# Performance work log

Hardware: AMD Instinct MI355X
Metric: run time of the kernel (lower is better)

The kernel has to match this reference:

```python
import jax, jax.numpy as jnp
import numpy as np

N_NODES = 100000
N_EDGES = 1600000
F_IN = 256
HID = 128
N_CLS = 64
K_APPNP = 10
ALPHA = 0.1


def setup_inputs() -> dict:
    key = jax.random.key(0)
    ks = jax.random.split(key, 12)
    x = jax.random.normal(ks[0], (N_NODES, F_IN), dtype=jnp.float32)
    edge_index = jax.random.randint(ks[1], (2, N_EDGES), 0, N_NODES, dtype=jnp.int64)
    def lin(k, fan_in, fan_out):
        s = 1.0 / np.sqrt(fan_in)
        kw, kb = jax.random.split(k)
        W = jax.random.uniform(kw, (fan_in, fan_out), minval=-s, maxval=s, dtype=jnp.float32)
        b = jax.random.uniform(kb, (fan_out,), minval=-s, maxval=s, dtype=jnp.float32)
        return W, b
    W1, b1 = lin(ks[2], F_IN, HID)
    W2, b2 = lin(ks[3], HID, HID)
    Wc, bc = lin(ks[4], HID, N_CLS)
    We, be = lin(ks[5], N_CLS, N_CLS)
    return {"x": x, "edge_index": edge_index, "W1": W1, "b1": b1, "W2": W2,
            "b2": b2, "Wc": Wc, "bc": bc, "We": We, "be": be}


def reference(x, edge_index, W1, b1, W2, b2, Wc, bc, We, be):
    N = x.shape[0]
    loop = jnp.arange(N)
    row = jnp.concatenate([edge_index[0], loop])  # source nodes (+ self loops)
    col = jnp.concatenate([edge_index[1], loop])  # target nodes (+ self loops)
    # symmetric GCN normalization: deg computed on targets
    deg = jax.ops.segment_sum(jnp.ones_like(col, dtype=x.dtype), col, num_segments=N)
    dinv = jnp.where(deg > 0, jax.lax.rsqrt(deg), 0.0)
    norm = dinv[row] * dinv[col]  # [E+N]

    def prop(h):  # normalized scatter-add aggregation
        return jax.ops.segment_sum(h[row] * norm[:, None], col, num_segments=N)

    # GCNConv: transform -> propagate -> bias (dropout is eval no-op)
    h = jax.nn.relu(prop(x @ W1) + b1)
    h = jax.nn.relu(prop(h @ W2) + b2)
    logits = h @ Wc + bc
    ev = jax.nn.relu(logits @ We + be)
    # APPNP: z_{k+1} = (1-alpha) * A_hat z_k + alpha * ev
    z = ev
    for _ in range(K_APPNP):
        z = (1.0 - ALPHA) * prop(z) + ALPHA * ev
    return jax.nn.log_softmax(z, axis=1)
```

## Files before the change

### kernel.cpp

```cpp
#include <hip/hip_runtime.h>
#include <hip/hip_fp16.h>


struct __align__(16) half8 { __half2 h[4]; };
typedef _Float16 f16x8 __attribute__((ext_vector_type(8)));
typedef float f32x4 __attribute__((ext_vector_type(4)));

__global__ __launch_bounds__(256) void k_init(int* deg, int N) {
    int i = blockIdx.x * 256 + threadIdx.x;
    if (i < N) deg[i] = 1;
}

__global__ __launch_bounds__(256) void k_count(const int* __restrict__ dst,
                                               int* deg, int* __restrict__ rank, int E) {
    int e = blockIdx.x * 256 + threadIdx.x;
    if (e < E) {
        int r = atomicAdd(&deg[dst[e]], 1);
        rank[e] = r - 1;
    }
}

__global__ __launch_bounds__(256) void k_scanA(const int* __restrict__ deg, int* bs, int N) {
    __shared__ int s[256];
    int t = threadIdx.x;
    int i = blockIdx.x * 256 + t;
    int c = (i < N) ? (deg[i] - 1) : 0;
    s[t] = c; __syncthreads();
    for (int o = 128; o > 0; o >>= 1) {
        if (t < o) s[t] += s[t + o];
        __syncthreads();
    }
    if (t == 0) bs[blockIdx.x] = s[0];
}

__global__ __launch_bounds__(512) void k_scanB(int* bs, int NB) {
    __shared__ int s[512];
    int t = threadIdx.x;
    int v = (t < NB) ? bs[t] : 0;
    s[t] = v; __syncthreads();
    for (int o = 1; o < 512; o <<= 1) {
        int u = (t >= o) ? s[t - o] : 0;
        __syncthreads();
        s[t] += u;
        __syncthreads();
    }
    if (t < NB) bs[t] = s[t] - v;
}

__global__ __launch_bounds__(256) void k_scanC(const int* __restrict__ deg, const int* __restrict__ bs,
                                               int* row_ptr, float* dinv, int N) {
    __shared__ int s[256];
    int t = threadIdx.x;
    int i = blockIdx.x * 256 + t;
    int c = (i < N) ? (deg[i] - 1) : 0;
    s[t] = c; __syncthreads();
    for (int o = 1; o < 256; o <<= 1) {
        int u = (t >= o) ? s[t - o] : 0;
        __syncthreads();
        s[t] += u;
        __syncthreads();
    }
    if (i < N) {
        int off = bs[blockIdx.x];
        row_ptr[i] = off + s[t] - c;
        dinv[i] = rsqrtf((float)deg[i]);
        if (i == N - 1) row_ptr[N] = off + s[t];
    }
}

__global__ __launch_bounds__(256) void k_fill(const int* __restrict__ src, const int* __restrict__ dst,
                                              const int* __restrict__ row_ptr,
                                              const int* __restrict__ rank,
                                              int* __restrict__ csr_src, int E) {
    int e = blockIdx.x * 256 + threadIdx.x;
    if (e < E) csr_src[row_ptr[dst[e]] + rank[e]] = src[e];
}

__global__ __launch_bounds__(256) void k_fuseW(const float* __restrict__ Wc,
                                               const float* __restrict__ bc,
                                               const float* __restrict__ We,
                                               const float* __restrict__ be,
                                               float* __restrict__ Wf,
                                               float* __restrict__ bf) {
    __shared__ float sWe[64 * 64];
    int tid = threadIdx.x;
    for (int i = tid; i < 64 * 64 / 4; i += 256)
        ((float4*)sWe)[i] = ((const float4*)We)[i];
    __syncthreads();
    for (int idx = tid; idx < 128 * 64; idx += 256) {
        int r = idx >> 6, c = idx & 63;
        float s = 0.f;
#pragma unroll 8
        for (int j = 0; j < 64; j++) s += Wc[r * 64 + j] * sWe[j * 64 + c];
        Wf[idx] = s;
    }
    if (tid < 64) {
        float s = be[tid];
#pragma unroll 8
        for (int j = 0; j < 64; j++) s += bc[j] * sWe[j * 64 + tid];
        bf[tid] = s;
    }
}

__global__ __launch_bounds__(256) void k_prepW(const float* __restrict__ W,
                                               __half* __restrict__ Wt, int K, int NCOL) {
    int idx = blockIdx.x * 256 + threadIdx.x;
    if (idx < NCOL * K) {
        int n = idx / K, k = idx % K;
        Wt[idx] = __float2half(W[k * NCOL + n]);
    }
}

template <int K, bool IN_F16>
__global__ __launch_bounds__(256) void k_mfma_gemm(const void* __restrict__ Xv,
                                                   const __half* __restrict__ Wt,
                                                   const float* __restrict__ dinv,
                                                   __half* __restrict__ Y, int N) {
    constexpr int NK = K / 32;
    const int tid = threadIdx.x;
    const int wave = tid >> 6, lane = tid & 63;
    const int m = lane & 15, quad = lane >> 4;
    const int rw = (wave & 1) * 16;
    const int cb = (wave >> 1) * 64;
    const int rowBase = blockIdx.x * 32;
    int rowA = rowBase + rw + m;
    if (rowA > N - 1) rowA = N - 1;

    const float*  xf = (const float*)Xv;
    const __half* xh = (const __half*)Xv;
    const long aOff = (long)rowA * K + quad * 8;

    f32x4 d[4];
#pragma unroll
    for (int ct = 0; ct < 4; ++ct) d[ct] = {0.f, 0.f, 0.f, 0.f};

    f16x8 a[2];
    float4 t0[2], t1[2];
    f16x8 b[2][4];

    if constexpr (IN_F16) {
        a[0] = *(const f16x8*)&xh[aOff];
    } else {
        t0[0] = *(const float4*)&xf[aOff];
        t1[0] = *(const float4*)&xf[aOff + 4];
    }
#pragma unroll
    for (int ct = 0; ct < 4; ++ct)
        b[0][ct] = *(const f16x8*)&Wt[(long)(cb + ct * 16 + m) * K + quad * 8];

#pragma unroll
    for (int kc = 0; kc < NK; ++kc) {
        const int cur = kc & 1, nxt = cur ^ 1;
        if (kc + 1 < NK) {
            const int k1 = (kc + 1) * 32;
            if constexpr (IN_F16) {
                a[nxt] = *(const f16x8*)&xh[aOff + k1];
            } else {
                t0[nxt] = *(const float4*)&xf[aOff + k1];
                t1[nxt] = *(const float4*)&xf[aOff + k1 + 4];
            }
#pragma unroll
            for (int ct = 0; ct < 4; ++ct)
                b[nxt][ct] = *(const f16x8*)&Wt[(long)(cb + ct * 16 + m) * K + k1 + quad * 8];
        }
        if constexpr (!IN_F16) {
            f16x8 av;
            av[0] = (_Float16)t0[cur].x; av[1] = (_Float16)t0[cur].y;
            av[2] = (_Float16)t0[cur].z; av[3] = (_Float16)t0[cur].w;
            av[4] = (_Float16)t1[cur].x; av[5] = (_Float16)t1[cur].y;
            av[6] = (_Float16)t1[cur].z; av[7] = (_Float16)t1[cur].w;
            a[cur] = av;
        }
#pragma unroll
        for (int ct = 0; ct < 4; ++ct)
            d[ct] = __builtin_amdgcn_mfma_f32_16x16x32_f16(a[cur], b[cur][ct], d[ct], 0, 0, 0);
    }

#pragma unroll
    for (int ct = 0; ct < 4; ++ct) {
        const int col = cb + ct * 16 + m;
#pragma unroll
        for (int reg = 0; reg < 4; ++reg) {
            const int row = rowBase + rw + quad * 4 + reg;
            if (row < N)
                Y[(long)row * 128 + col] = __float2half(d[ct][reg] * dinv[row]);
        }
    }
}

__global__ __launch_bounds__(256) void k_cls(const __half* __restrict__ H,
                                             const __half* __restrict__ Wft,
                                             const float* __restrict__ bf,
                                             const float* __restrict__ dinv,
                                             float* __restrict__ ev,
                                             __half* __restrict__ evs, int N) {
    const int tid = threadIdx.x;
    const int wave = tid >> 6, lane = tid & 63;
    const int m = lane & 15, quad = lane >> 4;
    const int rowT = blockIdx.x * 64 + wave * 16;
    int rowA = rowT + m;
    if (rowA > N - 1) rowA = N - 1;
    const long aOff = (long)rowA * 128 + quad * 8;

    f32x4 d[4];
#pragma unroll
    for (int ct = 0; ct < 4; ++ct) d[ct] = {0.f, 0.f, 0.f, 0.f};

    f16x8 a[2], b[2][4];
    a[0] = *(const f16x8*)&H[aOff];
#pragma unroll
    for (int ct = 0; ct < 4; ++ct)
        b[0][ct] = *(const f16x8*)&Wft[(long)(ct * 16 + m) * 128 + quad * 8];

#pragma unroll
    for (int kc = 0; kc < 4; ++kc) {
        const int cur = kc & 1, nxt = cur ^ 1;
        if (kc + 1 < 4) {
            const int k1 = (kc + 1) * 32;
            a[nxt] = *(const f16x8*)&H[aOff + k1];
#pragma unroll
            for (int ct = 0; ct < 4; ++ct)
                b[nxt][ct] = *(const f16x8*)&Wft[(long)(ct * 16 + m) * 128 + k1 + quad * 8];
        }
#pragma unroll
        for (int ct = 0; ct < 4; ++ct)
            d[ct] = __builtin_amdgcn_mfma_f32_16x16x32_f16(a[cur], b[cur][ct], d[ct], 0, 0, 0);
    }

#pragma unroll
    for (int ct = 0; ct < 4; ++ct) {
        const int col = ct * 16 + m;
#pragma unroll
        for (int reg = 0; reg < 4; ++reg) {
            const int row = rowT + quad * 4 + reg;
            if (row < N) {
                float v = fmaxf(d[ct][reg] + bf[col], 0.f);
                ev[(long)row * 64 + col] = v;
                evs[(long)row * 64 + col] = __float2half(v * dinv[row]);
            }
        }
    }
}

template <int F, int MODE>
__global__ __launch_bounds__(256) void k_prop2(const __half* __restrict__ tab,
                                               const int* __restrict__ row_ptr,
                                               const int* __restrict__ csr_src,
                                               const float* __restrict__ dinv,
                                               const float* __restrict__ bias,
                                               const void* __restrict__ evx,
                                               void* __restrict__ out, int N) {
    constexpr int LPE = F / 8;
    constexpr int S = 64 / LPE;
    int wave = threadIdx.x >> 6;
    int lane = threadIdx.x & 63;
    int node = blockIdx.x * 4 + wave;
    if (node >= N) return;
    int slot = lane / LPE;
    int fl = lane % LPE;
    const int2 se = *(const int2*)&row_ptr[node];
    int s = se.x, e = se.y;

    float acc[8], accB[8];
#pragma unroll
    for (int q = 0; q < 8; q++) { acc[q] = 0.f; accB[q] = 0.f; }

    int j = s + slot;
    int i0 = 0, i1 = 0;
    if (j < e) i0 = csr_src[j];
    if (j + S < e) i1 = csr_src[j + S];
    while (j + S < e) {
        const int jn = j + 2 * S;
        int n0 = 0, n1 = 0;
        if (jn < e) n0 = csr_src[jn];
        if (jn + S < e) n1 = csr_src[jn + S];
        const half8 a = *(const half8*)&tab[(long)i0 * F + 8 * fl];
        const half8 b = *(const half8*)&tab[(long)i1 * F + 8 * fl];
#pragma unroll
        for (int q = 0; q < 4; q++) {
            float2 fa = __half22float2(a.h[q]);
            float2 fb = __half22float2(b.h[q]);
            acc[2 * q] += fa.x; acc[2 * q + 1] += fa.y;
            accB[2 * q] += fb.x; accB[2 * q + 1] += fb.y;
        }
        i0 = n0; i1 = n1; j = jn;
    }
    if (j < e) {
        const half8 a = *(const half8*)&tab[(long)i0 * F + 8 * fl];
#pragma unroll
        for (int q = 0; q < 4; q++) {
            float2 fa = __half22float2(a.h[q]);
            acc[2 * q] += fa.x; acc[2 * q + 1] += fa.y;
        }
    }
    if (slot == 0) {
        const half8 a = *(const half8*)&tab[(long)node * F + 8 * fl];
#pragma unroll
        for (int q = 0; q < 4; q++) {
            float2 fa = __half22float2(a.h[q]);
            acc[2 * q] += fa.x; acc[2 * q + 1] += fa.y;
        }
    }
#pragma unroll
    for (int q = 0; q < 8; q++) acc[q] += accB[q];

#pragma unroll
    for (int off = LPE; off < 64; off <<= 1) {
#pragma unroll
        for (int q = 0; q < 8; q++) acc[q] += __shfl_xor(acc[q], off, 64);
    }

    if (slot == 0) {
        float di = dinv[node];
        if (MODE == 3) {
            const float4 b0 = *(const float4*)&bias[8 * fl];
            const float4 b1 = *(const float4*)&bias[8 * fl + 4];
            half8 ov;
            ov.h[0] = __floats2half2_rn(fmaxf(di * acc[0] + b0.x, 0.f),
                                        fmaxf(di * acc[1] + b0.y, 0.f));
            ov.h[1] = __floats2half2_rn(fmaxf(di * acc[2] + b0.z, 0.f),
                                        fmaxf(di * acc[3] + b0.w, 0.f));
            ov.h[2] = __floats2half2_rn(fmaxf(di * acc[4] + b1.x, 0.f),
                                        fmaxf(di * acc[5] + b1.y, 0.f));
            ov.h[3] = __floats2half2_rn(fmaxf(di * acc[6] + b1.z, 0.f),
                                        fmaxf(di * acc[7] + b1.w, 0.f));
            *(half8*)&((__half*)out)[(long)node * F + 8 * fl] = ov;
        } else if (MODE == 1) {
            float d2 = 0.9f * di * di;
            const half8 eh = *(const half8*)&((const __half*)evx)[(long)node * F + 8 * fl];
            half8 ov;
#pragma unroll
            for (int q = 0; q < 4; q++) {
                float2 ef = __half22float2(eh.h[q]);
                float vx = d2 * acc[2 * q] + 0.1f * ef.x;
                float vy = d2 * acc[2 * q + 1] + 0.1f * ef.y;
                ov.h[q] = __floats2half2_rn(vx, vy);
            }
            *(half8*)&((__half*)out)[(long)node * F + 8 * fl] = ov;
        } else {
            float d1 = 0.9f * di;
            const float* ef = (const float*)evx + (long)node * F + 8 * fl;
            const float4 e0 = *(const float4*)ef;
            const float4 e1 = *(const float4*)(ef + 4);
            float v[8];
            v[0] = d1 * acc[0] + 0.1f * e0.x;
            v[1] = d1 * acc[1] + 0.1f * e0.y;
            v[2] = d1 * acc[2] + 0.1f * e0.z;
            v[3] = d1 * acc[3] + 0.1f * e0.w;
            v[4] = d1 * acc[4] + 0.1f * e1.x;
            v[5] = d1 * acc[5] + 0.1f * e1.y;
            v[6] = d1 * acc[6] + 0.1f * e1.z;
            v[7] = d1 * acc[7] + 0.1f * e1.w;
            float m = v[0];
#pragma unroll
            for (int q = 1; q < 8; q++) m = fmaxf(m, v[q]);
#pragma unroll
            for (int off = 1; off < LPE; off <<= 1) m = fmaxf(m, __shfl_xor(m, off, 64));
            float ssum = 0.f;
#pragma unroll
            for (int q = 0; q < 8; q++) ssum += __expf(v[q] - m);
#pragma unroll
            for (int off = 1; off < LPE; off <<= 1) ssum += __shfl_xor(ssum, off, 64);
            float lse = m + __logf(ssum);
            float* o = (float*)out + (long)node * F + 8 * fl;
            float4 v0, v1;
            v0.x = v[0] - lse; v0.y = v[1] - lse; v0.z = v[2] - lse; v0.w = v[3] - lse;
            v1.x = v[4] - lse; v1.y = v[5] - lse; v1.z = v[6] - lse; v1.w = v[7] - lse;
            *(float4*)o = v0;
            *(float4*)(o + 4) = v1;
        }
    }
}

extern "C" void kernel_launch(void* const* d_in, const int* in_sizes, int n_in,
                              void* d_out, int out_size, void* d_ws, size_t ws_size,
                              hipStream_t stream) {
    const float* x  = (const float*)d_in[0];
    const int* edges = (const int*)d_in[1];
    const float* W1 = (const float*)d_in[2];
    const float* b1 = (const float*)d_in[3];
    const float* W2 = (const float*)d_in[4];
    const float* b2 = (const float*)d_in[5];
    const float* Wc = (const float*)d_in[6];
    const float* bc = (const float*)d_in[7];
    const float* We = (const float*)d_in[8];
    const float* be = (const float*)d_in[9];

    const int N = in_sizes[0] / 256;
    const int E = in_sizes[1] / 2;
    const int* esrc = edges;
    const int* edst = edges + E;

    char* ws = (char*)d_ws;
    size_t off = 0;
    auto alloc = [&](size_t bytes) -> void* {
        void* p = ws + off;
        off += (bytes + 255) & ~(size_t)255;
        return p;
    };
    int*    deg     = (int*)alloc((size_t)N * 4);
    int*    row_ptr = (int*)alloc((size_t)(N + 1) * 4);
    float*  dinv    = (float*)alloc((size_t)N * 4);
    int*    bs      = (int*)alloc(4096 * 4);
    int*    rank    = (int*)alloc((size_t)E * 4);
    int*    csr_src = (int*)alloc((size_t)E * 4);
    __half* P       = (__half*)alloc((size_t)N * 128 * 2);
    __half* Q16     = (__half*)alloc((size_t)N * 128 * 2);
    __half* zA      = (__half*)alloc((size_t)N * 64 * 2);
    __half* zB      = (__half*)alloc((size_t)N * 64 * 2);
    __half* evs     = (__half*)alloc((size_t)N * 64 * 2);
    float*  Wf      = (float*)alloc(128 * 64 * 4);
    float*  bf      = (float*)alloc(64 * 4);
    __half* W1t     = (__half*)alloc(128 * 256 * 2);
    __half* W2t     = (__half*)alloc(128 * 128 * 2);
    __half* Wft     = (__half*)alloc(64 * 128 * 2);
    float*  ev      = (float*)d_out;

    const int nbN = (N + 255) / 256;
    const int nbE = (E + 255) / 256;
    const int nbP = (N + 3) / 4;
    const int nbG = (N + 31) / 32;
    const int nbC = (N + 63) / 64;

    k_init<<<nbN, 256, 0, stream>>>(deg, N);
    k_count<<<nbE, 256, 0, stream>>>(edst, deg, rank, E);
    k_fuseW<<<1, 256, 0, stream>>>(Wc, bc, We, be, Wf, bf);
    k_prepW<<<(128 * 256 + 255) / 256, 256, 0, stream>>>(W1, W1t, 256, 128);
    k_prepW<<<(128 * 128 + 255) / 256, 256, 0, stream>>>(W2, W2t, 128, 128);
    k_prepW<<<(64 * 128 + 255) / 256, 256, 0, stream>>>(Wf, Wft, 128, 64);
    k_scanA<<<nbN, 256, 0, stream>>>(deg, bs, N);
    k_scanB<<<1, 512, 0, stream>>>(bs, nbN);
    k_scanC<<<nbN, 256, 0, stream>>>(deg, bs, row_ptr, dinv, N);
    k_fill<<<nbE, 256, 0, stream>>>(esrc, edst, row_ptr, rank, csr_src, E);

    k_mfma_gemm<256, false><<<nbG, 256, 0, stream>>>(x, W1t, dinv, P, N);
    k_prop2<128, 3><<<nbP, 256, 0, stream>>>(P, row_ptr, csr_src, dinv, b1, nullptr, Q16, N);

    k_mfma_gemm<128, true><<<nbG, 256, 0, stream>>>(Q16, W2t, dinv, P, N);
    k_prop2<128, 3><<<nbP, 256, 0, stream>>>(P, row_ptr, csr_src, dinv, b2, nullptr, Q16, N);

    k_cls<<<nbC, 256, 0, stream>>>(Q16, Wft, bf, dinv, ev, evs, N);

    const __half* zin = evs;
    __half* zout;
    for (int it = 0; it < 9; ++it) {
        zout = (it % 2 == 0) ? zA : zB;
        k_prop2<64, 1><<<nbP, 256, 0, stream>>>(zin, row_ptr, csr_src, dinv, nullptr, evs, zout, N);
        zin = zout;
    }
    k_prop2<64, 2><<<nbP, 256, 0, stream>>>(zin, row_ptr, csr_src, dinv, nullptr, ev, (float*)d_out, N);
}
```

Before: 1.030 ms.

## Stage weights in LDS with fragment-ordered layout and enlarge GEMM row tiles

Weight matrices are pre-permuted into an MFMA-fragment-ordered layout and loaded once per block into shared memory, instead of each wave re-reading them from global memory. The GEMM and classifier kernels now use 512-thread blocks covering 128 rows, with each wave computing all output columns for its 16 rows, and all A fragments are loaded up front. This aims to reduce redundant global weight traffic and improve latency hiding in the dense stages. In exchange it adds LDS use (up to 64KB for K=256) and more registers per thread, which may limit occupancy.

```diff
diff --git a/kernel.cpp b/kernel.cpp
--- a/kernel.cpp
+++ b/kernel.cpp
@@ -5,6 +5,13 @@
 struct __align__(16) half8 { __half2 h[4]; };
 typedef _Float16 f16x8 __attribute__((ext_vector_type(8)));
 typedef float f32x4 __attribute__((ext_vector_type(4)));
+
+__device__ __forceinline__ f16x8 cvt8(const float4& a, const float4& b) {
+    f16x8 r;
+    r[0] = (_Float16)a.x; r[1] = (_Float16)a.y; r[2] = (_Float16)a.z; r[3] = (_Float16)a.w;
+    r[4] = (_Float16)b.x; r[5] = (_Float16)b.y; r[6] = (_Float16)b.z; r[7] = (_Float16)b.w;
+    return r;
+}
 
 __global__ __launch_bounds__(256) void k_init(int* deg, int N) {
     int i = blockIdx.x * 256 + threadIdx.x;
@@ -102,129 +109,153 @@
     }
 }
 
-__global__ __launch_bounds__(256) void k_prepW(const float* __restrict__ W,
-                                               __half* __restrict__ Wt, int K, int NCOL) {
+__global__ __launch_bounds__(256) void k_prepW2(const float* __restrict__ W,
+                                                __half* __restrict__ Wt, int K, int NCOL) {
     int idx = blockIdx.x * 256 + threadIdx.x;
-    if (idx < NCOL * K) {
-        int n = idx / K, k = idx % K;
-        Wt[idx] = __float2half(W[k * NCOL + n]);
-    }
+    if (idx >= K * NCOL) return;
+    int j = idx & 7;
+    int n = (idx >> 3) % NCOL;
+    int qk = idx / (8 * NCOL);
+    int quad = qk & 3, kc = qk >> 2;
+    int k = kc * 32 + quad * 8 + j;
+    Wt[idx] = __float2half(W[k * NCOL + n]);
 }
 
 template <int K, bool IN_F16>
-__global__ __launch_bounds__(256) void k_mfma_gemm(const void* __restrict__ Xv,
-                                                   const __half* __restrict__ Wt,
-                                                   const float* __restrict__ dinv,
-                                                   __half* __restrict__ Y, int N) {
+__global__ __launch_bounds__(512, 4) void k_gemm(const void* __restrict__ Xv,
+                                                 const __half* __restrict__ Wtf,
+                                                 const float* __restrict__ dinv,
+                                                 __half* __restrict__ Y, int N) {
     constexpr int NK = K / 32;
+    constexpr int ITER = K / 32;
+    __shared__ __align__(16) __half sB[K * 128];
+
     const int tid = threadIdx.x;
-    const int wave = tid >> 6, lane = tid & 63;
-    const int m = lane & 15, quad = lane >> 4;
-    const int rw = (wave & 1) * 16;
-    const int cb = (wave >> 1) * 64;
-    const int rowBase = blockIdx.x * 32;
-    int rowA = rowBase + rw + m;
+    const int wv = tid >> 6, ln = tid & 63;
+    const int m = ln & 15, quad = ln >> 4;
+    const int rowBase = blockIdx.x * 128 + wv * 16;
+    int rowA = rowBase + m;
     if (rowA > N - 1) rowA = N - 1;
 
     const float*  xf = (const float*)Xv;
     const __half* xh = (const __half*)Xv;
     const long aOff = (long)rowA * K + quad * 8;
 
-    f32x4 d[4];
-#pragma unroll
-    for (int ct = 0; ct < 4; ++ct) d[ct] = {0.f, 0.f, 0.f, 0.f};
-
-    f16x8 a[2];
-    float4 t0[2], t1[2];
-    f16x8 b[2][4];
-
+    f16x8 a8[4];
+    float4 t0[4], t1[4];
     if constexpr (IN_F16) {
-        a[0] = *(const f16x8*)&xh[aOff];
+#pragma unroll
+        for (int kc = 0; kc < NK; ++kc)
+            a8[kc] = *(const f16x8*)&xh[aOff + kc * 32];
     } else {
-        t0[0] = *(const float4*)&xf[aOff];
-        t1[0] = *(const float4*)&xf[aOff + 4];
-    }
-#pragma unroll
-    for (int ct = 0; ct < 4; ++ct)
-        b[0][ct] = *(const f16x8*)&Wt[(long)(cb + ct * 16 + m) * K + quad * 8];
-
-#pragma unroll
-    for (int kc = 0; kc < NK; ++kc) {
-        const int cur = kc & 1, nxt = cur ^ 1;
-        if (kc + 1 < NK) {
-            const int k1 = (kc + 1) * 32;
-            if constexpr (IN_F16) {
-                a[nxt] = *(const f16x8*)&xh[aOff + k1];
-            } else {
-                t0[nxt] = *(const float4*)&xf[aOff + k1];
-                t1[nxt] = *(const float4*)&xf[aOff + k1 + 4];
+#pragma unroll
+        for (int c = 0; c < 4; ++c) {
+            t0[c] = *(const float4*)&xf[aOff + c * 32];
+            t1[c] = *(const float4*)&xf[aOff + c * 32 + 4];
+        }
+    }
+
+    {
+        f16x8 tb[ITER];
+        const f16x8* g = (const f16x8*)Wtf;
+#pragma unroll
+        for (int i = 0; i < ITER; ++i) tb[i] = g[(i * 8 + wv) * 64 + ln];
+        f16x8* l = (f16x8*)sB;
+#pragma unroll
+        for (int i = 0; i < ITER; ++i) l[(i * 8 + wv) * 64 + ln] = tb[i];
+    }
+    __syncthreads();
+
+    if constexpr (!IN_F16) {
+#pragma unroll
+        for (int c = 0; c < 4; ++c) a8[c] = cvt8(t0[c], t1[c]);
+#pragma unroll
+        for (int c = 0; c < 4; ++c) {
+            t0[c] = *(const float4*)&xf[aOff + (c + 4) * 32];
+            t1[c] = *(const float4*)&xf[aOff + (c + 4) * 32 + 4];
+        }
+    }
+
+    f32x4 d[8];
+#pragma unroll
+    for (int ct = 0; ct < 8; ++ct) d[ct] = {0.f, 0.f, 0.f, 0.f};
+
+#pragma unroll
+    for (int h = 0; h < NK / 4; ++h) {
+        if constexpr (!IN_F16) {
+            if (h == 1) {
+#pragma unroll
+                for (int c = 0; c < 4; ++c) a8[c] = cvt8(t0[c], t1[c]);
             }
-#pragma unroll
-            for (int ct = 0; ct < 4; ++ct)
-                b[nxt][ct] = *(const f16x8*)&Wt[(long)(cb + ct * 16 + m) * K + k1 + quad * 8];
-        }
-        if constexpr (!IN_F16) {
-            f16x8 av;
-            av[0] = (_Float16)t0[cur].x; av[1] = (_Float16)t0[cur].y;
-            av[2] = (_Float16)t0[cur].z; av[3] = (_Float16)t0[cur].w;
-            av[4] = (_Float16)t1[cur].x; av[5] = (_Float16)t1[cur].y;
-            av[6] = (_Float16)t1[cur].z; av[7] = (_Float16)t1[cur].w;
-            a[cur] = av;
-        }
-#pragma unroll
-        for (int ct = 0; ct < 4; ++ct)
-            d[ct] = __builtin_amdgcn_mfma_f32_16x16x32_f16(a[cur], b[cur][ct], d[ct], 0, 0, 0);
-    }
-
-#pragma unroll
-    for (int ct = 0; ct < 4; ++ct) {
-        const int col = cb + ct * 16 + m;
+        }
+#pragma unroll
+        for (int kq = 0; kq < 4; ++kq) {
+            const int kc = h * 4 + kq;
+            const f16x8 a = a8[IN_F16 ? kc : kq];
+            const __half* bb = &sB[(size_t)(kc * 4 + quad) * 128 * 8];
+#pragma unroll
+            for (int ct = 0; ct < 8; ++ct) {
+                const f16x8 b = *(const f16x8*)&bb[(ct * 16 + m) * 8];
+                d[ct] = __builtin_amdgcn_mfma_f32_16x16x32_f16(a, b, d[ct], 0, 0, 0);
+            }
+        }
+    }
+
+#pragma unroll
+    for (int ct = 0; ct < 8; ++ct) {
+        const int col = ct * 16 + m;
 #pragma unroll
         for (int reg = 0; reg < 4; ++reg) {
-            const int row = rowBase + rw + quad * 4 + reg;
+            const int row = rowBase + quad * 4 + reg;
             if (row < N)
                 Y[(long)row * 128 + col] = __float2half(d[ct][reg] * dinv[row]);
         }
     }
 }
 
-__global__ __launch_bounds__(256) void k_cls(const __half* __restrict__ H,
-                                             const __half* __restrict__ Wft,
-                                             const float* __restrict__ bf,
-                                             const float* __restrict__ dinv,
-                                             float* __restrict__ ev,
-                                             __half* __restrict__ evs, int N) {
+__global__ __launch_bounds__(512, 4) void k_cls(const __half* __restrict__ H,
+                                                const __half* __restrict__ Wtf,
+                                                const float* __restrict__ bf,
+                                                const float* __restrict__ dinv,
+                                                float* __restrict__ ev,
+                                                __half* __restrict__ evs, int N) {
+    __shared__ __align__(16) __half sB[128 * 64];
     const int tid = threadIdx.x;
-    const int wave = tid >> 6, lane = tid & 63;
-    const int m = lane & 15, quad = lane >> 4;
-    const int rowT = blockIdx.x * 64 + wave * 16;
-    int rowA = rowT + m;
+    const int wv = tid >> 6, ln = tid & 63;
+    const int m = ln & 15, quad = ln >> 4;
+    const int rowBase = blockIdx.x * 128 + wv * 16;
+    int rowA = rowBase + m;
     if (rowA > N - 1) rowA = N - 1;
     const long aOff = (long)rowA * 128 + quad * 8;
 
+    f16x8 a8[4];
+#pragma unroll
+    for (int kc = 0; kc < 4; ++kc)
+        a8[kc] = *(const f16x8*)&H[aOff + kc * 32];
+
+    {
+        f16x8 tb[2];
+        const f16x8* g = (const f16x8*)Wtf;
+#pragma unroll
+        for (int i = 0; i < 2; ++i) tb[i] = g[(i * 8 + wv) * 64 + ln];
+        f16x8* l = (f16x8*)sB;
+#pragma unroll
+        for (int i = 0; i < 2; ++i) l[(i * 8 + wv) * 64 + ln] = tb[i];
+    }
+    __syncthreads();
+
     f32x4 d[4];
 #pragma unroll
     for (int ct = 0; ct < 4; ++ct) d[ct] = {0.f, 0.f, 0.f, 0.f};
 
-    f16x8 a[2], b[2][4];
-    a[0] = *(const f16x8*)&H[aOff];
-#pragma unroll
-    for (int ct = 0; ct < 4; ++ct)
-        b[0][ct] = *(const f16x8*)&Wft[(long)(ct * 16 + m) * 128 + quad * 8];
-
 #pragma unroll
     for (int kc = 0; kc < 4; ++kc) {
-        const int cur = kc & 1, nxt = cur ^ 1;
-        if (kc + 1 < 4) {
-            const int k1 = (kc + 1) * 32;
-            a[nxt] = *(const f16x8*)&H[aOff + k1];
-#pragma unroll
-            for (int ct = 0; ct < 4; ++ct)
-                b[nxt][ct] = *(const f16x8*)&Wft[(long)(ct * 16 + m) * 128 + k1 + quad * 8];
-        }
-#pragma unroll
-        for (int ct = 0; ct < 4; ++ct)
-            d[ct] = __builtin_amdgcn_mfma_f32_16x16x32_f16(a[cur], b[cur][ct], d[ct], 0, 0, 0);
+        const __half* bb = &sB[(size_t)(kc * 4 + quad) * 64 * 8];
+#pragma unroll
+        for (int ct = 0; ct < 4; ++ct) {
+            const f16x8 b = *(const f16x8*)&bb[(ct * 16 + m) * 8];
+            d[ct] = __builtin_amdgcn_mfma_f32_16x16x32_f16(a8[kc], b, d[ct], 0, 0, 0);
+        }
     }
 
 #pragma unroll
@@ -232,7 +263,7 @@
         const int col = ct * 16 + m;
 #pragma unroll
         for (int reg = 0; reg < 4; ++reg) {
-            const int row = rowT + quad * 4 + reg;
+            const int row = rowBase + quad * 4 + reg;
             if (row < N) {
                 float v = fmaxf(d[ct][reg] + bf[col], 0.f);
                 ev[(long)row * 64 + col] = v;
@@ -419,27 +450,26 @@
     const int nbN = (N + 255) / 256;
     const int nbE = (E + 255) / 256;
     const int nbP = (N + 3) / 4;
-    const int nbG = (N + 31) / 32;
-    const int nbC = (N + 63) / 64;
+    const int TG  = (N + 127) / 128;
 
     k_init<<<nbN, 256, 0, stream>>>(deg, N);
     k_count<<<nbE, 256, 0, stream>>>(edst, deg, rank, E);
     k_fuseW<<<1, 256, 0, stream>>>(Wc, bc, We, be, Wf, bf);
-    k_prepW<<<(128 * 256 + 255) / 256, 256, 0, stream>>>(W1, W1t, 256, 128);
-    k_prepW<<<(128 * 128 + 255) / 256, 256, 0, stream>>>(W2, W2t, 128, 128);
-    k_prepW<<<(64 * 128 + 255) / 256, 256, 0, stream>>>(Wf, Wft, 128, 64);
+    k_prepW2<<<(256 * 128 + 255) / 256, 256, 0, stream>>>(W1, W1t, 256, 128);
+    k_prepW2<<<(128 * 128 + 255) / 256, 256, 0, stream>>>(W2, W2t, 128, 128);
+    k_prepW2<<<(128 * 64 + 255) / 256, 256, 0, stream>>>(Wf, Wft, 128, 64);
     k_scanA<<<nbN, 256, 0, stream>>>(deg, bs, N);
     k_scanB<<<1, 512, 0, stream>>>(bs, nbN);
     k_scanC<<<nbN, 256, 0, stream>>>(deg, bs, row_ptr, dinv, N);
     k_fill<<<nbE, 256, 0, stream>>>(esrc, edst, row_ptr, rank, csr_src, E);
 
-    k_mfma_gemm<256, false><<<nbG, 256, 0, stream>>>(x, W1t, dinv, P, N);
+    k_gemm<256, false><<<TG, 512, 0, stream>>>(x, W1t, dinv, P, N);
     k_prop2<128, 3><<<nbP, 256, 0, stream>>>(P, row_ptr, csr_src, dinv, b1, nullptr, Q16, N);
 
-    k_mfma_gemm<128, true><<<nbG, 256, 0, stream>>>(Q16, W2t, dinv, P, N);
+    k_gemm<128, true><<<TG, 512, 0, stream>>>(Q16, W2t, dinv, P, N);
     k_prop2<128, 3><<<nbP, 256, 0, stream>>>(P, row_ptr, csr_src, dinv, b2, nullptr, Q16, N);
 
-    k_cls<<<nbC, 256, 0, stream>>>(Q16, Wft, bf, dinv, ev, evs, N);
+    k_cls<<<TG, 512, 0, stream>>>(Q16, Wft, bf, dinv, ev, evs, N);
 
     const __half* zin = evs;
     __half* zout;
```

Result: faster. 972.3 us (-5.6%).
